# Performance work log

Measured on AMD Instinct MI355X. Metric: run time of the kernel, lower is better.

The kernel has to match this reference:

```python
import jax, jax.numpy as jnp
import numpy as np

N_NODE = 50000
D = 64
N_HEADS = 8
N_LAYERS = 2
NEG = -1e9
PAD = 0
STDV = 1.0 / np.sqrt(D)


def _l2norm(x, axis):
    n = jnp.sqrt(jnp.sum(x * x, axis=axis, keepdims=True))
    return x / jnp.maximum(n, 1e-12)


def _hgconv(x, theta, bias, edge_index):
    # PyG HypergraphConv (use_attention=False): out = D^-1 H B^-1 H^T (x @ theta) + bias
    xt = x @ theta
    node, hedge = edge_index[0], edge_index[1]
    ones = jnp.ones(node.shape[0], x.dtype)
    Bdeg = jax.ops.segment_sum(ones, hedge, num_segments=N_NODE)   # hyperedge degree
    Ddeg = jax.ops.segment_sum(ones, node, num_segments=N_NODE)    # node degree
    m = jax.ops.segment_sum(xt[node], hedge, num_segments=N_NODE)  # nodes -> hyperedges
    m = m * jnp.where(Bdeg > 0, 1.0 / Bdeg, 0.0)[:, None]
    out = jax.ops.segment_sum(m[hedge], node, num_segments=N_NODE) # hyperedges -> nodes
    out = out * jnp.where(Ddeg > 0, 1.0 / Ddeg, 0.0)[:, None]
    return out + bias


def _mha(x, w, pad_mask, reverse):
    # w: [4, D, D] -> q, k, v, out projections. reverse=True attends to future (triu).
    B, L, d = x.shape
    dk = d // N_HEADS
    split = lambda h: h.reshape(B, L, N_HEADS, dk).transpose(0, 2, 1, 3)
    q, k, v = split(x @ w[0]), split(x @ w[1]), split(x @ w[2])
    scores = jnp.einsum('bhid,bhjd->bhij', q, k) / jnp.sqrt(jnp.asarray(dk, x.dtype))
    tri = jnp.triu(jnp.ones((L, L), bool)) if reverse else jnp.tril(jnp.ones((L, L), bool))
    scores = jnp.where(tri[None, None], scores, NEG)
    scores = jnp.where(pad_mask[:, None, None, :], NEG, scores)
    attn = jax.nn.softmax(scores, axis=-1)
    out = jnp.einsum('bhij,bhjd->bhid', attn, v).transpose(0, 2, 1, 3).reshape(B, L, d)
    return out @ w[3], attn


def _prev_user_mask(seq):
    # scatter -1000 at every user id already seen up to position i (index 0 = PAD column)
    B, L = seq.shape
    tril = jnp.tril(jnp.ones((L, L), bool))
    idx = jnp.where(tril[None], seq[:, None, :], 0)                       # [B,L,L]
    idx = jnp.concatenate([idx, jnp.zeros((B, L, 1), idx.dtype)], axis=2)  # [B,L,L+1]
    b = jnp.arange(B)[:, None, None]
    i = jnp.arange(L)[None, :, None]
    return jnp.zeros((B, L, N_NODE), jnp.float32).at[b, i, idx].set(-1000.0)


def _hg_user(emb_table, gate_w, gate_b, att, att_m, theta, theta_b, edges):
    chans = []
    for c in range(3):
        x = emb_table * jax.nn.sigmoid(emb_table @ gate_w[c] + gate_b[c])  # self-gating
        acc, cur = x, x
        for k in range(N_LAYERS):
            cur = _hgconv(cur, theta[k], theta_b[k], edges[c])
            acc = acc + _l2norm(cur, axis=1)
        chans.append(acc / (N_LAYERS + 1))  # mean over [input, layer1, layer2]
    logits = jnp.stack([jnp.sum(att * (c @ att_m), axis=1) for c in chans], axis=1)  # [N,3]
    score = jax.nn.softmax(logits, axis=-1)
    return sum(score[:, i:i + 1] * chans[i] for i in range(3))


def setup_inputs() -> dict:
    key = jax.random.key(0)
    ks = jax.random.split(key, 20)
    u = lambda k, shp: jax.random.uniform(k, shp, jnp.float32, -STDV, STDV)
    B, L, E = 16, 50, 800000
    return {
        'input_seq': jax.random.randint(ks[0], (B, L), 0, N_NODE),
        'label_seq': jax.random.randint(ks[1], (B, L), 0, N_NODE),
        'input_time': jax.random.randint(ks[2], (B, L), 0, 100000),
        'label_time': jax.random.randint(ks[3], (B, L), 0, 100000),
        'edge_index_g': jax.random.randint(ks[4], (2, E), 0, N_NODE),
        'edge_index_i': jax.random.randint(ks[5], (2, E), 0, N_NODE),
        'edge_index_u': jax.random.randint(ks[6], (2, E), 0, N_NODE),
        'emb_table': u(ks[7], (N_NODE, D)),
        'gate_w': u(ks[8], (3, D, D)),
        'gate_b': u(ks[9], (3, D)),
        'att': u(ks[10], (D,)),
        'att_m': u(ks[11], (D, D)),
        'theta': u(ks[12], (N_LAYERS, D, D)),
        'theta_b': u(ks[13], (N_LAYERS, D)),
        'w_hist': u(ks[14], (4, D, D)),
        'w_fut': u(ks[15], (4, D, D)),
    }


def reference(input_seq, label_seq, input_time, label_time,
              edge_index_g, edge_index_i, edge_index_u,
              emb_table, gate_w, gate_b, att, att_m, theta, theta_b, w_hist, w_fut):
    # input_time / label_time are accepted but unused, as in the original forward.
    HG = _hg_user(emb_table, gate_w, gate_b, att, att_m, theta, theta_b,
                  (edge_index_g, edge_index_i, edge_index_u))
    pad_in = input_seq == PAD
    pad_lb = label_seq == PAD
    past_att_out, past_dist = _mha(HG[input_seq], w_hist, pad_in, reverse=False)
    fut_att_out, fut_dist = _mha(HG[label_seq], w_fut, pad_lb, reverse=True)
    output_past = (past_att_out @ HG.T + _prev_user_mask(input_seq)).reshape(-1, N_NODE)
    future_output = (fut_att_out @ HG.T).reshape(-1, N_NODE)
    return (output_past, future_output, past_dist, fut_dist,
            _l2norm(past_att_out, axis=1), _l2norm(fut_att_out, axis=1))
```

## Files before the change

### kernel.cpp

```cpp
#include <hip/hip_runtime.h>
#include <math.h>

#define N_NODE 50000
#define DD 64
#define NE 800000
#define BB 16
#define LL 50
#define NH 8
#define DK 8
#define NEGV -1e9f
#define NB 49
#define NBLK 256
#define EPB 3125

#define OFF_PDIST 80000000u
#define OFF_FDIST 80320000u
#define OFF_L2P 80640000u
#define OFF_L2F 80691200u

typedef unsigned short ushortt;
typedef __attribute__((ext_vector_type(8))) short bf16x8v;
typedef __attribute__((ext_vector_type(4))) float f32x4v;

__device__ __forceinline__ float b2f(ushortt h) { return __uint_as_float(((unsigned)h) << 16); }
__device__ __forceinline__ ushortt f2b(float f) {
    unsigned u = __float_as_uint(f);
    return (ushortt)((u + 0x7fffu + ((u >> 16) & 1u)) >> 16);
}
__device__ __forceinline__ void acc8(float* a, uint4 x) {
    a[0] += b2f((ushortt)(x.x)); a[1] += b2f((ushortt)(x.x >> 16));
    a[2] += b2f((ushortt)(x.y)); a[3] += b2f((ushortt)(x.y >> 16));
    a[4] += b2f((ushortt)(x.z)); a[5] += b2f((ushortt)(x.z >> 16));
    a[6] += b2f((ushortt)(x.w)); a[7] += b2f((ushortt)(x.w >> 16));
}
__device__ __forceinline__ uint4 pack8(const float* a) {
    uint4 w;
    w.x = (unsigned)f2b(a[0]) | ((unsigned)f2b(a[1]) << 16);
    w.y = (unsigned)f2b(a[2]) | ((unsigned)f2b(a[3]) << 16);
    w.z = (unsigned)f2b(a[4]) | ((unsigned)f2b(a[5]) << 16);
    w.w = (unsigned)f2b(a[6]) | ((unsigned)f2b(a[7]) << 16);
    return w;
}
__device__ __forceinline__ bool xcd_map(int bid, int& c, int& slot) {
    int r = bid & 7;
    c = (r * 3) >> 3;
    int nclass = (c == 2) ? 2 : 3;
    int base = (c == 0) ? 0 : ((c == 1) ? 3 : 6);
    slot = (bid >> 3) * nclass + (r - base);
    return slot < 12500;
}

__global__ void k_zero(float* p, int n) {
    int i = blockIdx.x * 256 + threadIdx.x;
    if (i < n) p[i] = 0.0f;
}

__global__ __launch_bounds__(256) void k_cnt(const int* __restrict__ eg,
                                             const int* __restrict__ ei,
                                             const int* __restrict__ eu,
                                             int* __restrict__ hist) {
    int c = blockIdx.y;
    const int* ed = (c == 0) ? eg : ((c == 1) ? ei : eu);
    int blk = blockIdx.x;
    __shared__ int lc[2 * NB];
    int tid = threadIdx.x;
    for (int j = tid; j < 2 * NB; j += 256) lc[j] = 0;
    __syncthreads();
    int e0 = blk * EPB;
    for (int i = e0 + tid; i < e0 + EPB; i += 256) {
        atomicAdd(&lc[ed[NE + i] >> 10], 1);
        atomicAdd(&lc[NB + (ed[i] >> 10)], 1);
    }
    __syncthreads();
    for (int j = tid; j < 2 * NB; j += 256) {
        int side = (j >= NB);
        int b = side ? (j - NB) : j;
        hist[(((side * 3 + c) * NB) + b) * NBLK + blk] = lc[j];
    }
}

__global__ __launch_bounds__(256) void k_scanH(int* __restrict__ hist, int* __restrict__ bb) {
    int t6 = blockIdx.x;
    int* h = hist + t6 * NB * NBLK;
    __shared__ int part[256];
    int tid = threadIdx.x;
    const int CH = (NB * NBLK) / 256;
    int base = tid * CH;
    int s = 0;
    for (int i = 0; i < CH; i++) s += h[base + i];
    part[tid] = s;
    __syncthreads();
    for (int o = 1; o < 256; o <<= 1) {
        int v = (tid >= o) ? part[tid - o] : 0;
        __syncthreads();
        part[tid] += v;
        __syncthreads();
    }
    int run = (tid == 0) ? 0 : part[tid - 1];
    for (int i = 0; i < CH; i++) {
        int idx = base + i;
        int v = h[idx];
        if ((idx & (NBLK - 1)) == 0) bb[t6 * (NB + 1) + (idx >> 8)] = run;
        h[idx] = run;
        run += v;
    }
    if (tid == 255) bb[t6 * (NB + 1) + NB] = run;
}

__global__ __launch_bounds__(256) void k_part2(const int* __restrict__ eg,
                                               const int* __restrict__ ei,
                                               const int* __restrict__ eu,
                                               const int* __restrict__ hist,
                                               unsigned* __restrict__ poolB,
                                               unsigned* __restrict__ poolD) {
    int c = blockIdx.y;
    const int* ed = (c == 0) ? eg : ((c == 1) ? ei : eu);
    int blk = blockIdx.x;
    __shared__ int curB[NB], curD[NB];
    int tid = threadIdx.x;
    for (int j = tid; j < NB; j += 256) {
        curB[j] = hist[(((0 * 3 + c) * NB) + j) * NBLK + blk];
        curD[j] = hist[(((1 * 3 + c) * NB) + j) * NBLK + blk];
    }
    __syncthreads();
    unsigned* pB = poolB + c * 800000;
    unsigned* pD = poolD + c * 800000;
    int e0 = blk * EPB;
    for (int i = e0 + tid; i < e0 + EPB; i += 256) {
        int n = ed[i], h = ed[NE + i];
        int pb = atomicAdd(&curB[h >> 10], 1);
        pB[pb] = ((unsigned)h << 16) | (unsigned)n;
        int pd = atomicAdd(&curD[n >> 10], 1);
        pD[pd] = ((unsigned)n << 16) | (unsigned)h;
    }
}

__global__ __launch_bounds__(256) void k_bucket(const unsigned* __restrict__ poolB,
                                                const unsigned* __restrict__ poolD,
                                                const int* __restrict__ bb,
                                                int* __restrict__ nbrB3, int* __restrict__ nbrD3,
                                                int* __restrict__ offB3, int* __restrict__ offD3,
                                                float* __restrict__ invB3, float* __restrict__ invD3) {
    int b = blockIdx.x, c = blockIdx.y, side = blockIdx.z;
    const unsigned* pool = (side ? poolD : poolB) + c * 800000;
    int* nbr = (side ? nbrD3 : nbrB3) + c * 800000;
    int* off = (side ? offD3 : offB3) + c * 50001;
    float* inv = (side ? invD3 : invB3) + c * 50000;
    int t6 = side * 3 + c;
    int s0 = bb[t6 * (NB + 1) + b], s1 = bb[t6 * (NB + 1) + b + 1];
    int baseSeg = b << 10;
    __shared__ int cnt[1024];
    __shared__ int ofs[1024];
    __shared__ int part[256];
    int tid = threadIdx.x;
    for (int j = tid; j < 1024; j += 256) cnt[j] = 0;
    __syncthreads();
    for (int i = s0 + tid; i < s1; i += 256)
        atomicAdd(&cnt[(pool[i] >> 16) & 1023], 1);
    __syncthreads();
    int t4 = tid * 4;
    int a0 = cnt[t4], a1 = cnt[t4 + 1], a2 = cnt[t4 + 2], a3 = cnt[t4 + 3];
    part[tid] = a0 + a1 + a2 + a3;
    __syncthreads();
    for (int o = 1; o < 256; o <<= 1) {
        int v = (tid >= o) ? part[tid - o] : 0;
        __syncthreads();
        part[tid] += v;
        __syncthreads();
    }
    int excl = (tid == 0) ? 0 : part[tid - 1];
    ofs[t4] = excl;
    ofs[t4 + 1] = excl + a0;
    ofs[t4 + 2] = excl + a0 + a1;
    ofs[t4 + 3] = excl + a0 + a1 + a2;
    __syncthreads();
    for (int ls = tid; ls < 1024; ls += 256) {
        int seg = baseSeg + ls;
        if (seg < N_NODE) {
            off[seg] = s0 + ofs[ls];
            inv[seg] = cnt[ls] ? 1.0f / (float)cnt[ls] : 0.0f;
        }
    }
    if (b == NB - 1 && tid == 0) off[N_NODE] = NE;
    __syncthreads();
    for (int i = s0 + tid; i < s1; i += 256) {
        unsigned u = pool[i];
        int ls = (u >> 16) & 1023;
        int p = atomicAdd(&ofs[ls], 1);
        nbr[s0 + p] = (int)(u & 0xFFFFu);
    }
}

__global__ __launch_bounds__(256) void k_gateX(const float* __restrict__ emb,
                                               const float* __restrict__ gate_w,
                                               const float* __restrict__ gate_b,
                                               float* __restrict__ acc3,
                                               ushortt* __restrict__ xt3) {
    int c = blockIdx.y;
    const float* W = gate_w + c * 4096;
    const float* bias = gate_b + c * 64;
    float* acc = acc3 + (size_t)c * 3200000;
    ushortt* xt = xt3 + (size_t)c * 3200000;
    __shared__ float sW[64 * 64];
    __shared__ float sx[4][64];
    int tid = threadIdx.x;
    for (int i = tid; i < 4096; i += 256) sW[i] = W[i];
    int r = tid >> 6;
    int d = tid & 63;
    int n = blockIdx.x * 4 + r;
    sx[r][d] = emb[n * DD + d];
    __syncthreads();
    float a = bias[d];
#pragma unroll
    for (int k = 0; k < 64; k++) a += sx[r][k] * sW[k * 64 + d];
    float x = sx[r][d] * (1.0f / (1.0f + expf(-a)));
    acc[n * DD + d] = x;
    xt[n * DD + d] = f2b(x);
}

__global__ __launch_bounds__(256) void k_gathB3(const ushortt* __restrict__ xt3,
                                                const int* __restrict__ offB3,
                                                const int* __restrict__ nbrB3,
                                                const float* __restrict__ invB3,
                                                ushortt* __restrict__ m3) {
    int c, slot;
    if (!xcd_map(blockIdx.x, c, slot)) return;
    const ushortt* src = xt3 + (size_t)c * 3200000;
    const int* off = offB3 + c * 50001;
    const int* nbr = nbrB3 + c * 800000;
    const float* invSeg = invB3 + c * 50000;
    ushortt* dst = m3 + (size_t)c * 3200000;
    int seg = slot * 4 + (threadIdx.x >> 6);
    int lane = threadIdx.x & 63;
    int sub = lane >> 3;
    int c8 = lane & 7;
    int s = off[seg], e = off[seg + 1];
    float a[8] = {0.f, 0.f, 0.f, 0.f, 0.f, 0.f, 0.f, 0.f};
    int i = s + sub;
    if (i < e) {
        uint4 x = ((const uint4*)(src + (size_t)nbr[i] * DD))[c8];
        for (i += 8; i < e; i += 8) {
            uint4 nx = ((const uint4*)(src + (size_t)nbr[i] * DD))[c8];
            acc8(a, x);
            x = nx;
        }
        acc8(a, x);
    }
#pragma unroll
    for (int j = 0; j < 8; j++) {
        a[j] += __shfl_xor(a[j], 8, 64);
        a[j] += __shfl_xor(a[j], 16, 64);
        a[j] += __shfl_xor(a[j], 32, 64);
    }
    if (sub == 0) {
        float sc = invSeg[seg];
        float b[8];
#pragma unroll
        for (int j = 0; j < 8; j++) b[j] = a[j] * sc;
        ((uint4*)(dst + (size_t)seg * DD))[c8] = pack8(b);
    }
}

template <int WRITE_XT>
__global__ __launch_bounds__(256) void k_gathD3f(const ushortt* __restrict__ m3,
                                                 const int* __restrict__ offD3,
                                                 const int* __restrict__ nbrD3,
                                                 const float* __restrict__ invD3,
                                                 const float* __restrict__ theta,
                                                 const float* __restrict__ theta_b,
                                                 float* __restrict__ acc3,
                                                 ushortt* __restrict__ xt3) {
    int c, slot;
    if (!xcd_map(blockIdx.x, c, slot)) return;
    const ushortt* m = m3 + (size_t)c * 3200000;
    const int* off = offD3 + c * 50001;
    const int* nbr = nbrD3 + c * 800000;
    const float* invD = invD3 + c * 50000;
    float* acc = acc3 + (size_t)c * 3200000;
    ushortt* xt = xt3 + (size_t)c * 3200000;

    __shared__ float sTh[64 * 64];
    __shared__ float sx[4][64];
    __shared__ float sb[64];
    int tid = threadIdx.x;
    for (int i = tid; i < 4096; i += 256) sTh[i] = theta[i];
    if (tid < 64) sb[tid] = theta_b[tid];

    int w = tid >> 6;
    int seg = slot * 4 + w;
    int lane = tid & 63;
    int sub = lane >> 3;
    int c8 = lane & 7;
    int s = off[seg], e = off[seg + 1];
    float a[8] = {0.f, 0.f, 0.f, 0.f, 0.f, 0.f, 0.f, 0.f};
    int i = s + sub;
    if (i < e) {
        uint4 x = ((const uint4*)(m + (size_t)nbr[i] * DD))[c8];
        for (i += 8; i < e; i += 8) {
            uint4 nx = ((const uint4*)(m + (size_t)nbr[i] * DD))[c8];
            acc8(a, x);
            x = nx;
        }
        acc8(a, x);
    }
#pragma unroll
    for (int j = 0; j < 8; j++) {
        a[j] += __shfl_xor(a[j], 8, 64);
        a[j] += __shfl_xor(a[j], 16, 64);
        a[j] += __shfl_xor(a[j], 32, 64);
    }
    if (sub == 0) {
        float iD = invD[seg];
#pragma unroll
        for (int j = 0; j < 8; j++) sx[w][c8 * 8 + j] = a[j] * iD;
    }
    __syncthreads();

    int d = lane;
    float v = sb[d];
#pragma unroll
    for (int k = 0; k < 64; k++) v += sx[w][k] * sTh[k * 64 + d];
    float ss = v * v;
#pragma unroll
    for (int o = 32; o; o >>= 1) ss += __shfl_xor(ss, o, 64);
    float nr = fmaxf(sqrtf(ss), 1e-12f);
    size_t idx = (size_t)seg * DD + d;
    acc[idx] += v / nr;
    if (WRITE_XT) xt[idx] = f2b(v);
}

__global__ __launch_bounds__(256) void k_comb(const float* __restrict__ a0,
                                              const float* __restrict__ a1,
                                              const float* __restrict__ a2,
                                              const float* __restrict__ att_m,
                                              const float* __restrict__ att,
                                              float* __restrict__ HG,
                                              ushortt* __restrict__ HG16) {
    __shared__ float svv[64];
    int tid = threadIdx.x;
    if (tid < 64) {
        float s = 0.f;
        for (int k = 0; k < 64; k++) s += att_m[tid * 64 + k] * att[k];
        svv[tid] = s;
    }
    __syncthreads();
    int r = tid >> 6;
    int d = tid & 63;
    int n = blockIdx.x * 4 + r;
    float x0 = a0[n * DD + d], x1 = a1[n * DD + d], x2 = a2[n * DD + d];
    float vd = svv[d];
    float l0 = x0 * vd, l1 = x1 * vd, l2 = x2 * vd;
#pragma unroll
    for (int o = 32; o; o >>= 1) {
        l0 += __shfl_xor(l0, o, 64);
        l1 += __shfl_xor(l1, o, 64);
        l2 += __shfl_xor(l2, o, 64);
    }
    l0 *= (1.0f / 3.0f); l1 *= (1.0f / 3.0f); l2 *= (1.0f / 3.0f);
    float mx = fmaxf(l0, fmaxf(l1, l2));
    float e0 = expf(l0 - mx), e1 = expf(l1 - mx), e2 = expf(l2 - mx);
    float inv = 1.0f / (e0 + e1 + e2);
    float hv = (e0 * x0 + e1 * x1 + e2 * x2) * inv * (1.0f / 3.0f);
    HG[n * DD + d] = hv;
    HG16[n * DD + d] = f2b(hv);
}

__global__ __launch_bounds__(256) void k_attnh(const float* __restrict__ HG,
                                               const int* __restrict__ iseq,
                                               const int* __restrict__ lseq,
                                               const float* __restrict__ w_hist,
                                               const float* __restrict__ w_fut,
                                               float* __restrict__ dout,
                                               float* __restrict__ hout) {
    int b = blockIdx.x, h = blockIdx.y, dir = blockIdx.z;
    const int* seq = dir ? lseq : iseq;
    const float* W = dir ? w_fut : w_hist;
    float* dist = dout + (dir ? OFF_FDIST : OFF_PDIST);
    __shared__ float sX[LL * 64];
    __shared__ float sQ[LL * DK], sK[LL * DK], sV[LL * DK];
    __shared__ float sS[LL * LL];
    __shared__ int sseq[LL];
    int tid = threadIdx.x, w = tid >> 6, lane = tid & 63;
    if (tid < LL) sseq[tid] = seq[b * LL + tid];
    __syncthreads();
    for (int idx = tid; idx < LL * 64; idx += 256)
        sX[idx] = HG[sseq[idx >> 6] * DD + (idx & 63)];
    __syncthreads();
    for (int idx = tid; idx < LL * DK; idx += 256) {
        int i = idx / DK, d = idx % DK;
        int col = h * 8 + d;
        float q = 0, k = 0, v = 0;
        for (int kk = 0; kk < 64; kk++) {
            float x = sX[i * 64 + kk];
            q += x * W[kk * 64 + col];
            k += x * W[4096 + kk * 64 + col];
            v += x * W[8192 + kk * 64 + col];
        }
        sQ[idx] = q; sK[idx] = k; sV[idx] = v;
    }
    __syncthreads();
    const float scale = 0.35355339059327373f;
    for (int idx = tid; idx < LL * LL; idx += 256) {
        int i = idx / LL, j = idx % LL;
        float s = 0;
#pragma unroll
        for (int d = 0; d < DK; d++) s += sQ[i * DK + d] * sK[j * DK + d];
        s *= scale;
        bool allowed = dir ? (j >= i) : (j <= i);
        if (!allowed || sseq[j] == 0) s = NEGV;
        sS[idx] = s;
    }
    __syncthreads();
    for (int i = w; i < LL; i += 4) {
        float v = (lane < LL) ? sS[i * LL + lane] : -INFINITY;
        float mx = v;
#pragma unroll
        for (int o = 32; o; o >>= 1) mx = fmaxf(mx, __shfl_xor(mx, o, 64));
        float e = (lane < LL) ? expf(v - mx) : 0.0f;
        float sum = e;
#pragma unroll
        for (int o = 32; o; o >>= 1) sum += __shfl_xor(sum, o, 64);
        float p = e / sum;
        if (lane < LL) {
            sS[i * LL + lane] = p;
            dist[((b * NH + h) * LL + i) * LL + lane] = p;
        }
    }
    __syncthreads();
    for (int idx = tid; idx < LL * DK; idx += 256) {
        int i = idx / DK, d = idx % DK;
        float o = 0;
        for (int j = 0; j < LL; j++) o += sS[i * LL + j] * sV[j * DK + d];
        hout[((size_t)(dir * 800 + b * LL + i)) * 64 + h * 8 + d] = o;
    }
}

__global__ __launch_bounds__(256) void k_attno(const float* __restrict__ hout,
                                               const float* __restrict__ w_hist,
                                               const float* __restrict__ w_fut,
                                               float* __restrict__ dout,
                                               ushortt* __restrict__ attout16) {
    int b = blockIdx.x, dir = blockIdx.y;
    const float* W = dir ? w_fut : w_hist;
    __shared__ float sH[LL * 64];
    __shared__ float sO[LL * 64];
    __shared__ float sInv[64];
    int tid = threadIdx.x;
    for (int idx = tid; idx < LL * 64; idx += 256)
        sH[idx] = hout[((size_t)(dir * 800 + b * LL)) * 64 + idx];
    __syncthreads();
    for (int idx = tid; idx < LL * 64; idx += 256) {
        int i = idx >> 6, d = idx & 63;
        float o = 0;
        for (int kk = 0; kk < 64; kk++) o += sH[i * 64 + kk] * W[3 * 4096 + kk * 64 + d];
        sO[idx] = o;
        int row = dir * 800 + b * LL + i;
        attout16[row * 64 + d] = f2b(o);
    }
    __syncthreads();
    if (tid < 64) {
        float s = 0;
        for (int l = 0; l < LL; l++) {
            float x = sO[l * 64 + tid];
            s += x * x;
        }
        sInv[tid] = 1.0f / fmaxf(sqrtf(s), 1e-12f);
    }
    __syncthreads();
    float* ol2 = dout + (dir ? OFF_L2F : OFF_L2P) + b * LL * 64;
    for (int idx = tid; idx < LL * 64; idx += 256) ol2[idx] = sO[idx] * sInv[idx & 63];
}

__global__ __launch_bounds__(256) void k_bigmm_mfma(const ushortt* __restrict__ A16,
                                                    const ushortt* __restrict__ HG16,
                                                    float* __restrict__ out) {
    __shared__ float sO[16][260];
    int tid = threadIdx.x;
    int lane = tid & 63;
    int w = tid >> 6;
    int rt = blockIdx.y;
    int colBase = blockIdx.x * 256;
    int lrow = lane & 15;
    int kb = (lane >> 4) * 8;
    int arow = rt * 16 + lrow;
    bf16x8v a0 = *(const bf16x8v*)(A16 + (size_t)arow * 64 + kb);
    bf16x8v a1 = *(const bf16x8v*)(A16 + (size_t)arow * 64 + kb + 32);
#pragma unroll
    for (int ct = 0; ct < 4; ct++) {
        int lc = w * 64 + ct * 16 + lrow;
        int col = colBase + lc;
        int colc = (col < N_NODE) ? col : 0;
        bf16x8v b0 = *(const bf16x8v*)(HG16 + (size_t)colc * 64 + kb);
        bf16x8v b1 = *(const bf16x8v*)(HG16 + (size_t)colc * 64 + kb + 32);
        f32x4v acc = {0.f, 0.f, 0.f, 0.f};
        acc = __builtin_amdgcn_mfma_f32_16x16x32_bf16(a0, b0, acc, 0, 0, 0);
        acc = __builtin_amdgcn_mfma_f32_16x16x32_bf16(a1, b1, acc, 0, 0, 0);
        int r0 = (lane >> 4) * 4;
#pragma unroll
        for (int j = 0; j < 4; j++) sO[r0 + j][lc] = acc[j];
    }
    __syncthreads();
#pragma unroll
    for (int j = 0; j < 4; j++) {
        int r = w * 4 + j;
        int row = rt * 16 + r;
        int c0 = colBase + lane * 4;
        f32x4v v = {sO[r][lane * 4], sO[r][lane * 4 + 1],
                    sO[r][lane * 4 + 2], sO[r][lane * 4 + 3]};
        if (c0 + 3 < N_NODE) {
            __builtin_nontemporal_store(v, (f32x4v*)(out + (size_t)row * 50000 + c0));
        } else {
            for (int t = 0; t < 4; t++)
                if (c0 + t < N_NODE) out[(size_t)row * 50000 + c0 + t] = v[t];
        }
    }
}

__global__ __launch_bounds__(64) void k_mask(const int* __restrict__ iseq,
                                             float* __restrict__ out) {
    int row = blockIdx.x;
    int b = row / LL, i = row % LL;
    __shared__ int s[LL];
    int tid = threadIdx.x;
    if (tid < LL) s[tid] = iseq[b * LL + tid];
    __syncthreads();
    float* o = out + (size_t)row * 50000;
    if (tid == 0) o[0] -= 1000.0f;
    if (tid < LL && tid <= i) {
        int c = s[tid];
        if (c > 0 && c < N_NODE) {
            bool first = true;
            for (int j = 0; j < tid; j++)
                if (s[j] == c) { first = false; break; }
            if (first) o[c] -= 1000.0f;
        }
    }
}

__global__ void k_deg(const int* __restrict__ node, const int* __restrict__ hedge,
                      float* __restrict__ Ddeg, float* __restrict__ Bdeg) {
    int e = blockIdx.x * 256 + threadIdx.x;
    if (e < NE) {
        atomicAdd(&Ddeg[node[e]], 1.0f);
        atomicAdd(&Bdeg[hedge[e]], 1.0f);
    }
}

__global__ void k_inv(float* a, int n) {
    int i = blockIdx.x * 256 + threadIdx.x;
    if (i < n) a[i] = (a[i] > 0.0f) ? (1.0f / a[i]) : 0.0f;
}

__global__ __launch_bounds__(256) void k_scat(const float* __restrict__ src,
                                              const int* __restrict__ gidx,
                                              const int* __restrict__ sidx,
                                              const float* __restrict__ scale,
                                              float* __restrict__ dst) {
    int e = blockIdx.x * 4 + (threadIdx.x >> 6);
    int d = threadIdx.x & 63;
    if (e >= NE) return;
    int g = gidx[e];
    int s = sidx[e];
    float v = src[g * DD + d];
    if (scale) v *= scale[g];
    atomicAdd(&dst[s * DD + d], v);
}

__global__ __launch_bounds__(256) void k_fin(float* __restrict__ cur,
                                             const float* __restrict__ invD,
                                             const float* __restrict__ bias,
                                             float* __restrict__ acc) {
    int r = threadIdx.x >> 6;
    int d = threadIdx.x & 63;
    int n = blockIdx.x * 4 + r;
    float v = cur[n * DD + d] * invD[n] + bias[d];
    cur[n * DD + d] = v;
    float s = v * v;
#pragma unroll
    for (int o = 32; o; o >>= 1) s += __shfl_xor(s, o, 64);
    float nr = fmaxf(sqrtf(s), 1e-12f);
    acc[n * DD + d] += v / nr;
}

__global__ __launch_bounds__(256) void k_gate(const float* __restrict__ emb,
                                              const float* __restrict__ W,
                                              const float* __restrict__ bias,
                                              float* __restrict__ cur,
                                              float* __restrict__ acc) {
    __shared__ float sW[64 * 64];
    __shared__ float sx[4][64];
    int tid = threadIdx.x;
    for (int i = tid; i < 4096; i += 256) sW[i] = W[i];
    int r = tid >> 6;
    int d = tid & 63;
    int n = blockIdx.x * 4 + r;
    sx[r][d] = emb[n * DD + d];
    __syncthreads();
    float a = bias[d];
#pragma unroll
    for (int k = 0; k < 64; k++) a += sx[r][k] * sW[k * 64 + d];
    float x = sx[r][d] * (1.0f / (1.0f + expf(-a)));
    cur[n * DD + d] = x;
    acc[n * DD + d] = x;
}

__global__ __launch_bounds__(256) void k_mm64(const float* __restrict__ X,
                                              const float* __restrict__ W,
                                              float* __restrict__ Y) {
    __shared__ float sW[64 * 64];
    __shared__ float sx[4][64];
    int tid = threadIdx.x;
    for (int i = tid; i < 4096; i += 256) sW[i] = W[i];
    int r = tid >> 6;
    int d = tid & 63;
    int n = blockIdx.x * 4 + r;
    sx[r][d] = X[n * DD + d];
    __syncthreads();
    float a = 0.0f;
#pragma unroll
    for (int k = 0; k < 64; k++) a += sx[r][k] * sW[k * 64 + d];
    Y[n * DD + d] = a;
}

__global__ __launch_bounds__(256) void k_attnF(const float* __restrict__ HG,
                                               const int* __restrict__ iseq,
                                               const int* __restrict__ lseq,
                                               const float* __restrict__ w_hist,
                                               const float* __restrict__ w_fut,
                                               float* __restrict__ dout,
                                               float* __restrict__ attoutF) {
    int b = blockIdx.x;
    int dir = blockIdx.y;
    const int* seq = (dir == 0) ? iseq : lseq;
    const float* W = (dir == 0) ? w_hist : w_fut;
    float* dist = dout + ((dir == 0) ? OFF_PDIST : OFF_FDIST);
    __shared__ float sX[LL * 64];
    __shared__ float sQ[LL * 64];
    __shared__ float sK[LL * 64];
    __shared__ float sV[LL * 64];
    __shared__ float sS[LL * LL];
    __shared__ float sInv[64];
    __shared__ int sseq[LL];
    int tid = threadIdx.x;
    int w = tid >> 6, lane = tid & 63;
    if (tid < LL) sseq[tid] = seq[b * LL + tid];
    __syncthreads();
    for (int idx = tid; idx < LL * 64; idx += 256) {
        int i = idx >> 6, d = idx & 63;
        sX[idx] = HG[sseq[i] * DD + d];
    }
    __syncthreads();
    for (int idx = tid; idx < LL * 64; idx += 256) {
        int i = idx >> 6, d = idx & 63;
        float q = 0, k = 0, v = 0;
        for (int kk = 0; kk < 64; kk++) {
            float x = sX[i * 64 + kk];
            q += x * W[kk * 64 + d];
            k += x * W[4096 + kk * 64 + d];
            v += x * W[8192 + kk * 64 + d];
        }
        sQ[idx] = q; sK[idx] = k; sV[idx] = v;
    }
    __syncthreads();
    for (int idx = tid; idx < LL * 64; idx += 256) sX[idx] = 0.0f;
    __syncthreads();
    const float scale = 0.35355339059327373f;
    for (int h = 0; h < NH; h++) {
        for (int idx = tid; idx < LL * LL; idx += 256) {
            int i = idx / LL, j = idx % LL;
            float s = 0;
#pragma unroll
            for (int d = 0; d < DK; d++) s += sQ[i * 64 + h * 8 + d] * sK[j * 64 + h * 8 + d];
            s *= scale;
            bool allowed = (dir == 0) ? (j <= i) : (j >= i);
            if (!allowed || sseq[j] == 0) s = NEGV;
            sS[idx] = s;
        }
        __syncthreads();
        for (int i = w; i < LL; i += 4) {
            float v = (lane < LL) ? sS[i * LL + lane] : -INFINITY;
            float mx = v;
#pragma unroll
            for (int o = 32; o; o >>= 1) mx = fmaxf(mx, __shfl_xor(mx, o, 64));
            float e = (lane < LL) ? expf(v - mx) : 0.0f;
            float sum = e;
#pragma unroll
            for (int o = 32; o; o >>= 1) sum += __shfl_xor(sum, o, 64);
            float p = e / sum;
            if (lane < LL) {
                sS[i * LL + lane] = p;
                dist[((b * NH + h) * LL + i) * LL + lane] = p;
            }
        }
        __syncthreads();
        for (int idx = tid; idx < LL * DK; idx += 256) {
            int i = idx / DK, d8 = idx % DK;
            float o = 0;
            for (int j = 0; j < LL; j++) o += sS[i * LL + j] * sV[j * 64 + h * 8 + d8];
            sX[i * 64 + h * 8 + d8] = o;
        }
        __syncthreads();
    }
    for (int idx = tid; idx < LL * 64; idx += 256) {
        int i = idx >> 6, d = idx & 63;
        float o = 0;
        for (int kk = 0; kk < 64; kk++) o += sX[i * 64 + kk] * W[3 * 4096 + kk * 64 + d];
        sQ[idx] = o;
        attoutF[(dir * 800 + b * LL + i) * 64 + d] = o;
    }
    __syncthreads();
    if (tid < 64) {
        float s = 0;
        for (int l = 0; l < LL; l++) {
            float x = sQ[l * 64 + tid];
            s += x * x;
        }
        sInv[tid] = 1.0f / fmaxf(sqrtf(s), 1e-12f);
    }
    __syncthreads();
    float* ol2 = dout + ((dir == 0) ? OFF_L2P : OFF_L2F) + b * LL * 64;
    for (int idx = tid; idx < LL * 64; idx += 256) {
        int d = idx & 63;
        ol2[idx] = sQ[idx] * sInv[d];
    }
}

__global__ __launch_bounds__(256) void k_bigmm5(const float* __restrict__ A,
                                                const float* __restrict__ HG,
                                                float* __restrict__ out) {
    int col = blockIdx.x * 256 + threadIdx.x;
    int r0 = blockIdx.y * 400;
    bool ok = (col < N_NODE);
    float4 h[16];
    const float4* hp = (const float4*)(HG + (size_t)(ok ? col : 0) * 64);
#pragma unroll
    for (int t = 0; t < 16; t++) h[t] = hp[t];
    if (!ok) return;
    for (int r = 0; r < 400; r++) {
        int row = r0 + r;
        const float* ar = A + (size_t)row * 64;
        float q0 = 0.f, q1 = 0.f, q2 = 0.f, q3 = 0.f;
#pragma unroll
        for (int t = 0; t < 16; t++) {
            q0 += ar[4 * t + 0] * h[t].x;
            q1 += ar[4 * t + 1] * h[t].y;
            q2 += ar[4 * t + 2] * h[t].z;
            q3 += ar[4 * t + 3] * h[t].w;
        }
        out[(size_t)row * 50000 + col] = (q0 + q1) + (q2 + q3);
    }
}

extern "C" void kernel_launch(void* const* d_in, const int* in_sizes, int n_in,
                              void* d_out, int out_size, void* d_ws, size_t ws_size,
                              hipStream_t stream) {
    const int* input_seq = (const int*)d_in[0];
    const int* label_seq = (const int*)d_in[1];
    const int* eg = (const int*)d_in[4];
    const int* ei = (const int*)d_in[5];
    const int* eu = (const int*)d_in[6];
    const float* emb = (const float*)d_in[7];
    const float* gate_w = (const float*)d_in[8];
    const float* gate_b = (const float*)d_in[9];
    const float* att = (const float*)d_in[10];
    const float* att_m = (const float*)d_in[11];
    const float* theta = (const float*)d_in[12];
    const float* theta_b = (const float*)d_in[13];
    const float* w_hist = (const float*)d_in[14];
    const float* w_fut = (const float*)d_in[15];

    float* out = (float*)d_out;
    float* ws = (float*)d_ws;

    const size_t HGF = 3200000;
    const int HISTN = 6 * NB * NBLK;
    const size_t needA = (HGF + 150000 + 150000 +
                          (size_t)(HISTN + 6 * (NB + 1) + 64) +
                          300006 + 4 * 2400000 +
                          2 * 2400000 +
                          3 * HGF +
                          HGF / 2 + 51200 + 102400 + 1024) * 4;

    if (ws_size >= needA) {
        size_t o = 0;
        float* HG = ws + o; o += HGF;
        float* invB3 = ws + o; o += 150000;
        float* invD3 = ws + o; o += 150000;
        int* hist = (int*)(ws + o); o += HISTN;
        int* bbarr = (int*)(ws + o); o += 6 * (NB + 1) + 64;
        int* offB3 = (int*)(ws + o); o += 150003;
        int* offD3 = (int*)(ws + o); o += 150003 + 2;
        int* nbrB3 = (int*)(ws + o); o += 2400000;
        int* nbrD3 = (int*)(ws + o); o += 2400000;
        unsigned* poolB = (unsigned*)(ws + o); o += 2400000;
        unsigned* poolD = (unsigned*)(ws + o); o += 2400000;
        ushortt* xt3 = (ushortt*)(ws + o); o += 4800000;
        ushortt* m3 = (ushortt*)(ws + o); o += 4800000;
        float* acc3 = ws + o; o += 3 * HGF;
        ushortt* HG16 = (ushortt*)(ws + o); o += HGF / 2;
        ushortt* A16 = (ushortt*)(ws + o); o += 51200;
        float* hout = ws + o; o += 102400;

        dim3 pg(NBLK, 3);
        k_cnt<<<pg, 256, 0, stream>>>(eg, ei, eu, hist);
        k_scanH<<<6, 256, 0, stream>>>(hist, bbarr);
        k_part2<<<pg, 256, 0, stream>>>(eg, ei, eu, hist, poolB, poolD);
        dim3 dg(NB, 3, 2);
        k_bucket<<<dg, 256, 0, stream>>>(poolB, poolD, bbarr, nbrB3, nbrD3,
                                         offB3, offD3, invB3, invD3);

        dim3 ng3(12500, 3);
        k_gateX<<<ng3, 256, 0, stream>>>(emb, gate_w, gate_b, acc3, xt3);
        k_gathB3<<<50000, 256, 0, stream>>>(xt3, offB3, nbrB3, invB3, m3);
        k_gathD3f<1><<<50000, 256, 0, stream>>>(m3, offD3, nbrD3, invD3,
                                                theta, theta_b, acc3, xt3);
        k_gathB3<<<50000, 256, 0, stream>>>(xt3, offB3, nbrB3, invB3, m3);
        k_gathD3f<0><<<50000, 256, 0, stream>>>(m3, offD3, nbrD3, invD3,
                                                theta + 4096, theta_b + 64, acc3, xt3);

        k_comb<<<12500, 256, 0, stream>>>(acc3, acc3 + HGF, acc3 + 2 * HGF,
                                          att_m, att, HG, HG16);
        dim3 ah(BB, NH, 2);
        k_attnh<<<ah, 256, 0, stream>>>(HG, input_seq, label_seq, w_hist, w_fut, out, hout);
        dim3 ao(BB, 2);
        k_attno<<<ao, 256, 0, stream>>>(hout, w_hist, w_fut, out, A16);
        dim3 bg(196, 100);
        k_bigmm_mfma<<<bg, 256, 0, stream>>>(A16, HG16, out);
        k_mask<<<BB * LL, 64, 0, stream>>>(input_seq, out);
    } else {
        float* HG = ws;
        float* invB = HG + HGF;
        float* invD = invB + 50000;
        if (ws_size < (HGF + 100000 + 64) * 4) {
            HG = out + 36550000u;
            invB = HG + HGF;
            invD = invB + 50000;
        }
        float* trans = out;
        float* acc0 = trans;
        float* acc1 = trans + HGF;
        float* acc2 = trans + 2 * HGF;
        float* cur = trans + 3 * HGF;
        float* xt = trans + 4 * HGF;
        float* m = trans + 5 * HGF;
        float* accs[3] = {acc0, acc1, acc2};
        const int* edges[3] = {eg, ei, eu};
        for (int c = 0; c < 3; c++) {
            const int* node = edges[c];
            const int* hedge = edges[c] + NE;
            k_zero<<<(100000 + 255) / 256, 256, 0, stream>>>(invB, 100000);
            k_deg<<<(NE + 255) / 256, 256, 0, stream>>>(node, hedge, invD, invB);
            k_inv<<<(100000 + 255) / 256, 256, 0, stream>>>(invB, 100000);
            k_gate<<<12500, 256, 0, stream>>>(emb, gate_w + c * 4096, gate_b + c * 64, cur, accs[c]);
            for (int k = 0; k < 2; k++) {
                k_mm64<<<12500, 256, 0, stream>>>(cur, theta + k * 4096, xt);
                k_zero<<<12500, 256, 0, stream>>>(m, (int)HGF);
                k_scat<<<NE / 4, 256, 0, stream>>>(xt, node, hedge, nullptr, m);
                k_zero<<<12500, 256, 0, stream>>>(cur, (int)HGF);
                k_scat<<<NE / 4, 256, 0, stream>>>(m, hedge, node, invB, cur);
                k_fin<<<12500, 256, 0, stream>>>(cur, invD, theta_b + k * 64, accs[c]);
            }
        }
        k_comb<<<12500, 256, 0, stream>>>(acc0, acc1, acc2, att_m, att, HG, (ushortt*)m);
        dim3 ag(BB, 2);
        k_attnF<<<ag, 256, 0, stream>>>(HG, input_seq, label_seq, w_hist, w_fut, out, xt);
        dim3 bg5(196, 4);
        k_bigmm5<<<bg5, 256, 0, stream>>>(xt, HG, out);
        k_mask<<<BB * LL, 64, 0, stream>>>(input_seq, out);
    }
}
```

Before: 867.0 us.

## Split hypergraph gathers into column halves and move theta transform to separate kernel

Each gather pass now handles only 32 of the 64 feature columns, so the randomly gathered source table per graph is half as large and more likely to stay in the per-XCD L2. The index loads and the output stores use nontemporal hints so streaming data does not evict the gathered rows. The theta projection, normalisation and accumulation move out of the node-side gather into a separate dense kernel. The cost is more launches and an extra round trip through memory for the aggregated features.

```diff
diff --git a/kernel.cpp b/kernel.cpp
--- a/kernel.cpp
+++ b/kernel.cpp
@@ -21,6 +21,7 @@
 typedef unsigned short ushortt;
 typedef __attribute__((ext_vector_type(8))) short bf16x8v;
 typedef __attribute__((ext_vector_type(4))) float f32x4v;
+typedef __attribute__((ext_vector_type(4))) unsigned int u32x4v;
 
 __device__ __forceinline__ float b2f(ushortt h) { return __uint_as_float(((unsigned)h) << 16); }
 __device__ __forceinline__ ushortt f2b(float f) {
@@ -218,29 +219,32 @@
     xt[n * DD + d] = f2b(x);
 }
 
-__global__ __launch_bounds__(256) void k_gathB3(const ushortt* __restrict__ xt3,
-                                                const int* __restrict__ offB3,
-                                                const int* __restrict__ nbrB3,
-                                                const float* __restrict__ invB3,
-                                                ushortt* __restrict__ m3) {
+__global__ __launch_bounds__(256) void k_gathH(const ushortt* __restrict__ srcb,
+                                               const int* __restrict__ off3,
+                                               const int* __restrict__ nbr3,
+                                               const float* __restrict__ inv3,
+                                               ushortt* __restrict__ dstb,
+                                               int half) {
     int c, slot;
     if (!xcd_map(blockIdx.x, c, slot)) return;
-    const ushortt* src = xt3 + (size_t)c * 3200000;
-    const int* off = offB3 + c * 50001;
-    const int* nbr = nbrB3 + c * 800000;
-    const float* invSeg = invB3 + c * 50000;
-    ushortt* dst = m3 + (size_t)c * 3200000;
+    const ushortt* src = srcb + (size_t)c * 3200000 + half * 32;
+    ushortt* dst = dstb + (size_t)c * 3200000 + half * 32;
+    const int* off = off3 + c * 50001;
+    const int* nbr = nbr3 + c * 800000;
+    const float* inv = inv3 + c * 50000;
     int seg = slot * 4 + (threadIdx.x >> 6);
     int lane = threadIdx.x & 63;
-    int sub = lane >> 3;
-    int c8 = lane & 7;
+    int sub = lane >> 2;
+    int c4 = lane & 3;
     int s = off[seg], e = off[seg + 1];
     float a[8] = {0.f, 0.f, 0.f, 0.f, 0.f, 0.f, 0.f, 0.f};
     int i = s + sub;
     if (i < e) {
-        uint4 x = ((const uint4*)(src + (size_t)nbr[i] * DD))[c8];
-        for (i += 8; i < e; i += 8) {
-            uint4 nx = ((const uint4*)(src + (size_t)nbr[i] * DD))[c8];
+        int nb = __builtin_nontemporal_load(&nbr[i]);
+        uint4 x = ((const uint4*)(src + (size_t)nb * DD))[c4];
+        for (i += 16; i < e; i += 16) {
+            int nb2 = __builtin_nontemporal_load(&nbr[i]);
+            uint4 nx = ((const uint4*)(src + (size_t)nb2 * DD))[c4];
             acc8(a, x);
             x = nx;
         }
@@ -248,85 +252,53 @@
     }
 #pragma unroll
     for (int j = 0; j < 8; j++) {
+        a[j] += __shfl_xor(a[j], 4, 64);
         a[j] += __shfl_xor(a[j], 8, 64);
         a[j] += __shfl_xor(a[j], 16, 64);
         a[j] += __shfl_xor(a[j], 32, 64);
     }
     if (sub == 0) {
-        float sc = invSeg[seg];
+        float sc = inv[seg];
         float b[8];
 #pragma unroll
         for (int j = 0; j < 8; j++) b[j] = a[j] * sc;
-        ((uint4*)(dst + (size_t)seg * DD))[c8] = pack8(b);
+        u32x4v w;
+        w.x = (unsigned)f2b(b[0]) | ((unsigned)f2b(b[1]) << 16);
+        w.y = (unsigned)f2b(b[2]) | ((unsigned)f2b(b[3]) << 16);
+        w.z = (unsigned)f2b(b[4]) | ((unsigned)f2b(b[5]) << 16);
+        w.w = (unsigned)f2b(b[6]) | ((unsigned)f2b(b[7]) << 16);
+        __builtin_nontemporal_store(w, (u32x4v*)(dst + (size_t)seg * DD) + c4);
     }
 }
 
 template <int WRITE_XT>
-__global__ __launch_bounds__(256) void k_gathD3f(const ushortt* __restrict__ m3,
-                                                 const int* __restrict__ offD3,
-                                                 const int* __restrict__ nbrD3,
-                                                 const float* __restrict__ invD3,
-                                                 const float* __restrict__ theta,
-                                                 const float* __restrict__ theta_b,
-                                                 float* __restrict__ acc3,
-                                                 ushortt* __restrict__ xt3) {
-    int c, slot;
-    if (!xcd_map(blockIdx.x, c, slot)) return;
-    const ushortt* m = m3 + (size_t)c * 3200000;
-    const int* off = offD3 + c * 50001;
-    const int* nbr = nbrD3 + c * 800000;
-    const float* invD = invD3 + c * 50000;
+__global__ __launch_bounds__(256) void k_theta(ushortt* __restrict__ t3,
+                                               const float* __restrict__ theta,
+                                               const float* __restrict__ theta_b,
+                                               float* __restrict__ acc3) {
+    int c = blockIdx.y;
+    ushortt* t = t3 + (size_t)c * 3200000;
     float* acc = acc3 + (size_t)c * 3200000;
-    ushortt* xt = xt3 + (size_t)c * 3200000;
-
-    __shared__ float sTh[64 * 64];
+    __shared__ float sTh[4096];
     __shared__ float sx[4][64];
     __shared__ float sb[64];
     int tid = threadIdx.x;
     for (int i = tid; i < 4096; i += 256) sTh[i] = theta[i];
     if (tid < 64) sb[tid] = theta_b[tid];
-
-    int w = tid >> 6;
-    int seg = slot * 4 + w;
-    int lane = tid & 63;
-    int sub = lane >> 3;
-    int c8 = lane & 7;
-    int s = off[seg], e = off[seg + 1];
-    float a[8] = {0.f, 0.f, 0.f, 0.f, 0.f, 0.f, 0.f, 0.f};
-    int i = s + sub;
-    if (i < e) {
-        uint4 x = ((const uint4*)(m + (size_t)nbr[i] * DD))[c8];
-        for (i += 8; i < e; i += 8) {
-            uint4 nx = ((const uint4*)(m + (size_t)nbr[i] * DD))[c8];
-            acc8(a, x);
-            x = nx;
-        }
-        acc8(a, x);
-    }
-#pragma unroll
-    for (int j = 0; j < 8; j++) {
-        a[j] += __shfl_xor(a[j], 8, 64);
-        a[j] += __shfl_xor(a[j], 16, 64);
-        a[j] += __shfl_xor(a[j], 32, 64);
-    }
-    if (sub == 0) {
-        float iD = invD[seg];
-#pragma unroll
-        for (int j = 0; j < 8; j++) sx[w][c8 * 8 + j] = a[j] * iD;
-    }
-    __syncthreads();
-
-    int d = lane;
+    int r = tid >> 6, d = tid & 63;
+    int n = blockIdx.x * 4 + r;
+    sx[r][d] = b2f(t[(size_t)n * DD + d]);
+    __syncthreads();
     float v = sb[d];
 #pragma unroll
-    for (int k = 0; k < 64; k++) v += sx[w][k] * sTh[k * 64 + d];
+    for (int k = 0; k < 64; k++) v += sx[r][k] * sTh[k * 64 + d];
     float ss = v * v;
 #pragma unroll
     for (int o = 32; o; o >>= 1) ss += __shfl_xor(ss, o, 64);
     float nr = fmaxf(sqrtf(ss), 1e-12f);
-    size_t idx = (size_t)seg * DD + d;
+    size_t idx = (size_t)n * DD + d;
     acc[idx] += v / nr;
-    if (WRITE_XT) xt[idx] = f2b(v);
+    if (WRITE_XT) t[idx] = f2b(v);
 }
 
 __global__ __launch_bounds__(256) void k_comb(const float* __restrict__ a0,
@@ -811,12 +783,16 @@
 
         dim3 ng3(12500, 3);
         k_gateX<<<ng3, 256, 0, stream>>>(emb, gate_w, gate_b, acc3, xt3);
-        k_gathB3<<<50000, 256, 0, stream>>>(xt3, offB3, nbrB3, invB3, m3);
-        k_gathD3f<1><<<50000, 256, 0, stream>>>(m3, offD3, nbrD3, invD3,
-                                                theta, theta_b, acc3, xt3);
-        k_gathB3<<<50000, 256, 0, stream>>>(xt3, offB3, nbrB3, invB3, m3);
-        k_gathD3f<0><<<50000, 256, 0, stream>>>(m3, offD3, nbrD3, invD3,
-                                                theta + 4096, theta_b + 64, acc3, xt3);
+        for (int k = 0; k < 2; k++) {
+            k_gathH<<<50000, 256, 0, stream>>>(xt3, offB3, nbrB3, invB3, m3, 0);
+            k_gathH<<<50000, 256, 0, stream>>>(xt3, offB3, nbrB3, invB3, m3, 1);
+            k_gathH<<<50000, 256, 0, stream>>>(m3, offD3, nbrD3, invD3, xt3, 0);
+            k_gathH<<<50000, 256, 0, stream>>>(m3, offD3, nbrD3, invD3, xt3, 1);
+            if (k == 0)
+                k_theta<1><<<ng3, 256, 0, stream>>>(xt3, theta, theta_b, acc3);
+            else
+                k_theta<0><<<ng3, 256, 0, stream>>>(xt3, theta + 4096, theta_b + 64, acc3);
+        }
 
         k_comb<<<12500, 256, 0, stream>>>(acc3, acc3 + HGF, acc3 + 2 * HGF,
                                           att_m, att, HG, HG16);
```

New measurement: 1.188 ms. 37.0% more time.
